# Performance work log

Measured on AMD Instinct MI355X. Metric: run time of the kernel, lower is better.

The kernel has to match this reference:

```python
import jax, jax.numpy as jnp
import numpy as np

EPS = 1e-5  # BatchNorm eps

def _bn(x):
    # BatchNorm1d(affine=False) in training mode: per-agent, per-feature batch stats
    m = jnp.mean(x, axis=1, keepdims=True)
    v = jnp.var(x, axis=1, keepdims=True)
    return (x - m) / jnp.sqrt(v + EPS)

def _lrelu(x):
    return jax.nn.leaky_relu(x, 0.01)

def setup_inputs() -> dict:
    key = jax.random.key(0)
    ks = jax.random.split(key, 14)
    A, B, IN, OUT, H, K = 8, 32768, 128, 32, 128, 4
    D = H // K
    s = 0.05
    return {
        "states": jax.random.normal(ks[0], (A, B, IN), jnp.float32),
        "actions": jax.random.normal(ks[1], (A, B, OUT), jnp.float32),
        "enc_w": jax.random.normal(ks[2], (A, IN + OUT, H), jnp.float32) * s,
        "enc_b": jax.random.normal(ks[3], (A, H), jnp.float32) * s,
        "aenc_w": jax.random.normal(ks[4], (A, OUT, H), jnp.float32) * s,
        "aenc_b": jax.random.normal(ks[5], (A, H), jnp.float32) * s,
        "key_w": jax.random.normal(ks[6], (K, H, D), jnp.float32) * s,
        "sel_w": jax.random.normal(ks[7], (K, H, D), jnp.float32) * s,
        "val_w": jax.random.normal(ks[8], (K, H, D), jnp.float32) * s,
        "val_b": jax.random.normal(ks[9], (K, D), jnp.float32) * s,
        "c1_w": jax.random.normal(ks[10], (A, 2 * H, H), jnp.float32) * s,
        "c1_b": jax.random.normal(ks[11], (A, H), jnp.float32) * s,
        "c2_w": jax.random.normal(ks[12], (A, H, 1), jnp.float32) * s,
        "c2_b": jax.random.normal(ks[13], (A, 1), jnp.float32) * s,
    }

def reference(states, actions, enc_w, enc_b, aenc_w, aenc_b,
              key_w, sel_w, val_w, val_b, c1_w, c1_b, c2_w, c2_b):
    A, B, _ = states.shape
    # per-agent state-action encodings: [A,B,H]
    sa = _bn(jnp.concatenate([states, actions], axis=-1))
    sa_enc = _lrelu(jnp.einsum('abi,aih->abh', sa, enc_w) + enc_b[:, None, :])
    # per-agent action encodings: [A,B,H]
    a_in = _bn(actions)
    a_enc = _lrelu(jnp.einsum('abi,aih->abh', a_in, aenc_w) + aenc_b[:, None, :])
    # per-head keys/values/selectors: [K,A,B,D]
    keys = jnp.einsum('abh,khd->kabd', a_enc, key_w)
    vals = _lrelu(jnp.einsum('abh,khd->kabd', a_enc, val_w) + val_b[:, None, None, :])
    sels = jnp.einsum('abh,khd->kabd', sa_enc, sel_w)
    D = keys.shape[-1]
    # attention logits over other agents: [K,B,A_query,A_key], self excluded
    logits = jnp.einsum('kibd,kjbd->kbij', sels, keys) / jnp.sqrt(jnp.float32(D))
    self_mask = jnp.eye(A, dtype=bool)[None, None]
    probs = jax.nn.softmax(jnp.where(self_mask, -jnp.inf, logits), axis=-1)
    # attended values: [K,A,B,D] -> concat heads -> [A,B,K*D]
    other = jnp.einsum('kbij,kjbd->kibd', probs, vals)
    other_cat = jnp.transpose(other, (1, 2, 0, 3)).reshape(A, B, -1)
    # per-agent critics on [sa_enc, attended]: [A,B,1]
    critic_in = jnp.concatenate([sa_enc, other_cat], axis=-1)
    h = _lrelu(jnp.einsum('abi,aih->abh', critic_in, c1_w) + c1_b[:, None, :])
    q = jnp.einsum('abh,aho->abo', h, c2_w) + c2_b[:, None, :]
    return q
```

## Files before the change

kernel.cpp:

```cpp
#include <hip/hip_runtime.h>
#include <hip/hip_bf16.h>
#include <stdint.h>

#define A_N 8
#define B_N 32768
#define IN_N 128
#define OUT_N 32
#define SAF 160
#define H_N 128
#define D_N 32
#define KD_N 128
#define CIN_N 256
#define CHUNKS 128
#define EPSV 1e-5f
#define ENC_KP 192

typedef unsigned int u32;
typedef unsigned short u16;
typedef __attribute__((ext_vector_type(8))) short short8;
typedef __attribute__((ext_vector_type(4))) float floatx4;

__device__ __forceinline__ float bf_lo(u32 u){ return __uint_as_float(u << 16); }
__device__ __forceinline__ float bf_hi(u32 u){ return __uint_as_float(u & 0xffff0000u); }
__device__ __forceinline__ float bf2f(u16 b){ return __uint_as_float(((u32)b) << 16); }
__device__ __forceinline__ u16 f2bf(float f){
  u32 u = __float_as_uint(f);
  return (u16)((u + 0x7fffu + ((u >> 16) & 1u)) >> 16);
}
__device__ __forceinline__ float lrelu(float x){ return x > 0.f ? x : 0.01f * x; }

__global__ __launch_bounds__(256) void k_stats(
    const float* __restrict__ states, const float* __restrict__ actions,
    float* __restrict__ part)
{
  int a = blockIdx.y;
  int chunk = blockIdx.x;
  int t = threadIdx.x;
  int r0 = chunk * (B_N / CHUNKS);
  __shared__ float red[512];
  {
    int f = t & 127, half = t >> 7;
    const float* p = states + ((size_t)a * B_N + r0 + half) * IN_N + f;
    float s1 = 0.f, s2 = 0.f;
    for (int it = 0; it < 128; ++it){
      float v = p[(size_t)(2 * it) * IN_N];
      s1 += v; s2 += v * v;
    }
    red[t] = s1; red[256 + t] = s2;
    __syncthreads();
    if (t < 128){
      float a1 = red[t] + red[t + 128];
      float a2 = red[256 + t] + red[256 + t + 128];
      size_t o = (((size_t)a * CHUNKS + chunk) * SAF + t) * 2;
      part[o] = a1; part[o + 1] = a2;
    }
    __syncthreads();
  }
  {
    int f = t & 31, g = t >> 5;
    const float* p = actions + ((size_t)a * B_N + r0 + g) * OUT_N + f;
    float s1 = 0.f, s2 = 0.f;
    for (int it = 0; it < 32; ++it){
      float v = p[(size_t)(8 * it) * OUT_N];
      s1 += v; s2 += v * v;
    }
    red[t] = s1; red[256 + t] = s2;
    __syncthreads();
    if (t < 32){
      float a1 = 0.f, a2 = 0.f;
      #pragma unroll
      for (int gg = 0; gg < 8; ++gg){
        a1 += red[t + 32 * gg];
        a2 += red[256 + t + 32 * gg];
      }
      size_t o = (((size_t)a * CHUNKS + chunk) * SAF + 128 + t) * 2;
      part[o] = a1; part[o + 1] = a2;
    }
  }
}

__global__ void k_finalize(const float* __restrict__ part,
                           float* __restrict__ meanArr, float* __restrict__ istdArr)
{
  int idx = blockIdx.x * blockDim.x + threadIdx.x;
  if (idx >= A_N * SAF) return;
  int a = idx / SAF, f = idx % SAF;
  float s1 = 0.f, s2 = 0.f;
  for (int c = 0; c < CHUNKS; ++c){
    size_t o = (((size_t)a * CHUNKS + c) * SAF + f) * 2;
    s1 += part[o]; s2 += part[o + 1];
  }
  float m = s1 * (1.f / B_N);
  float v = s2 * (1.f / B_N) - m * m;
  if (v < 0.f) v = 0.f;
  meanArr[idx] = m;
  istdArr[idx] = rsqrtf(v + EPSV);
}

__device__ __forceinline__ void packpair(float w, u16* __restrict__ dh,
                                         u16* __restrict__ dl, int i){
  u16 h = f2bf(w);
  dh[i] = h;
  dl[i] = f2bf(w - bf2f(h));
}

__global__ __launch_bounds__(256) void k_pack(
    const float* __restrict__ enc_w, const float* __restrict__ aenc_w,
    const float* __restrict__ key_w, const float* __restrict__ sel_w,
    const float* __restrict__ val_w, const float* __restrict__ c1_w,
    u16* __restrict__ encH, u16* __restrict__ encL,
    u16* __restrict__ aencH, u16* __restrict__ aencL,
    u16* __restrict__ keyH, u16* __restrict__ selH, u16* __restrict__ valH,
    u16* __restrict__ c1H, u16* __restrict__ c1L)
{
  int i = blockIdx.x * 256 + threadIdx.x;
  const int S0 = A_N * H_N * ENC_KP;
  const int S1 = A_N * H_N * OUT_N;
  const int S2 = KD_N * H_N;
  const int S5 = A_N * H_N * CIN_N;
  if (i < S0){
    int a = i / (H_N * ENC_KP); int r = i % (H_N * ENC_KP);
    int n = r / ENC_KP; int k = r % ENC_KP;
    float v = (k < SAF) ? enc_w[((size_t)a * SAF + k) * H_N + n] : 0.f;
    packpair(v, encH, encL, i);
    return;
  }
  i -= S0;
  if (i < S1){
    int a = i / (H_N * OUT_N); int r = i % (H_N * OUT_N);
    int n = r / OUT_N; int k = r % OUT_N;
    packpair(aenc_w[((size_t)a * OUT_N + k) * H_N + n], aencH, aencL, i);
    return;
  }
  i -= S1;
  if (i < 3 * S2){
    int which = i / S2; int j = i % S2;
    int n = j / H_N, k = j % H_N;
    const float* w = (which == 0) ? key_w : ((which == 1) ? sel_w : val_w);
    u16* dh = (which == 0) ? keyH : ((which == 1) ? selH : valH);
    dh[j] = f2bf(w[(((size_t)(n >> 5)) * H_N + k) * D_N + (n & 31)]);
    return;
  }
  i -= 3 * S2;
  if (i < S5){
    int a = i / (H_N * CIN_N); int r = i % (H_N * CIN_N);
    int n = r / CIN_N; int k = r % CIN_N;
    packpair(c1_w[((size_t)a * CIN_N + k) * H_N + n], c1H, c1L, i);
  }
}
#define PACK_TOTAL (A_N*H_N*ENC_KP + A_N*H_N*OUT_N + 3*KD_N*H_N + A_N*H_N*CIN_N)

__global__ __launch_bounds__(256, 3) void k_enc_sel(
    const float* __restrict__ states, const float* __restrict__ actions,
    const float* __restrict__ mean, const float* __restrict__ istd,
    const u16* __restrict__ encH, const u16* __restrict__ encL,
    const float* __restrict__ enc_b,
    const u16* __restrict__ selH,
    u16* __restrict__ sa_enc, u16* __restrict__ sels)
{
  int a = blockIdx.y; int row0 = blockIdx.x * 128; int t = threadIdx.x;
  int lane = t & 63, wave = t >> 6, l16 = lane & 15, quad = lane >> 4;
  __shared__ __align__(16) u16 S[22528];
  __shared__ __align__(16) float sc[192], sh[192];
  u16* Wh = S;
  u16* Wl = S + 5120;
  u16* Xh = S + 10240;
  u16* Xl = S + 15360;
  u16* T  = S;
  u16* Ws = S + 17408;

  if (t < 192){
    float m = 0.f, s = 0.f;
    if (t < SAF){ m = mean[a * SAF + t]; s = istd[a * SAF + t]; }
    sc[t] = s; sh[t] = -m * s;
  }
  floatx4 acc[2][8];
  #pragma unroll
  for (int mt = 0; mt < 2; ++mt)
    #pragma unroll
    for (int nt = 0; nt < 8; ++nt) acc[mt][nt] = (floatx4){0.f,0.f,0.f,0.f};
  const u16* wbh = encH + (size_t)a * H_N * ENC_KP;
  const u16* wbl = encL + (size_t)a * H_N * ENC_KP;
  __syncthreads();

  for (int k0 = 0; k0 < ENC_KP; k0 += 32){
    for (int c = t; c < 512; c += 256){
      int n = c >> 2, off = (c & 3) * 8;
      *(uint4*)&Wh[n * 40 + off] = *(const uint4*)(wbh + (size_t)n * ENC_KP + k0 + off);
      *(uint4*)&Wl[n * 40 + off] = *(const uint4*)(wbl + (size_t)n * ENC_KP + k0 + off);
    }
    for (int c = t; c < 1024; c += 256){
      int r = c >> 3, kc = (c & 7) * 4, f = k0 + kc;
      size_t row = (size_t)a * B_N + row0 + r;
      float4 v = {0.f, 0.f, 0.f, 0.f};
      if (f < IN_N)     v = *(const float4*)(states + row * IN_N + f);
      else if (f < SAF) v = *(const float4*)(actions + row * OUT_N + (f - IN_N));
      float4 scv = *(const float4*)&sc[f];
      float4 shv = *(const float4*)&sh[f];
      float x0 = fmaf(v.x, scv.x, shv.x), x1 = fmaf(v.y, scv.y, shv.y);
      float x2 = fmaf(v.z, scv.z, shv.z), x3 = fmaf(v.w, scv.w, shv.w);
      u16 h0 = f2bf(x0), h1 = f2bf(x1), h2 = f2bf(x2), h3 = f2bf(x3);
      *(u32*)&Xh[r * 40 + kc]     = (u32)h0 | ((u32)h1 << 16);
      *(u32*)&Xh[r * 40 + kc + 2] = (u32)h2 | ((u32)h3 << 16);
      u16 l0 = f2bf(x0 - bf2f(h0)), l1 = f2bf(x1 - bf2f(h1));
      u16 l2 = f2bf(x2 - bf2f(h2)), l3 = f2bf(x3 - bf2f(h3));
      *(u32*)&Xl[r * 40 + kc]     = (u32)l0 | ((u32)l1 << 16);
      *(u32*)&Xl[r * 40 + kc + 2] = (u32)l2 | ((u32)l3 << 16);
    }
    __syncthreads();
    {
      short8 ah[2], al[2], bh[8], bl[8];
      #pragma unroll
      for (int mt = 0; mt < 2; ++mt){
        int rr = (wave * 32 + mt * 16 + l16) * 40 + quad * 8;
        ah[mt] = *(const short8*)&Xh[rr];
        al[mt] = *(const short8*)&Xl[rr];
      }
      #pragma unroll
      for (int nt = 0; nt < 8; ++nt){
        int rr = (nt * 16 + l16) * 40 + quad * 8;
        bh[nt] = *(const short8*)&Wh[rr];
        bl[nt] = *(const short8*)&Wl[rr];
      }
      #pragma unroll
      for (int mt = 0; mt < 2; ++mt)
        #pragma unroll
        for (int nt = 0; nt < 8; ++nt){
          acc[mt][nt] = __builtin_amdgcn_mfma_f32_16x16x32_bf16(ah[mt], bh[nt], acc[mt][nt], 0,0,0);
          acc[mt][nt] = __builtin_amdgcn_mfma_f32_16x16x32_bf16(ah[mt], bl[nt], acc[mt][nt], 0,0,0);
          acc[mt][nt] = __builtin_amdgcn_mfma_f32_16x16x32_bf16(al[mt], bh[nt], acc[mt][nt], 0,0,0);
        }
    }
    __syncthreads();
  }

  {
    float bv[8];
    #pragma unroll
    for (int nt = 0; nt < 8; ++nt) bv[nt] = enc_b[a * H_N + nt * 16 + l16];
    #pragma unroll
    for (int mt = 0; mt < 2; ++mt)
      #pragma unroll
      for (int nt = 0; nt < 8; ++nt)
        #pragma unroll
        for (int r = 0; r < 4; ++r){
          int rl = wave * 32 + mt * 16 + quad * 4 + r;
          T[rl * 136 + nt * 16 + l16] = f2bf(lrelu(acc[mt][nt][r] + bv[nt]));
        }
  }
  __syncthreads();
  for (int c = t; c < 2048; c += 256){
    int row = c >> 4, col8 = (c & 15) * 8;
    *(uint4*)(sa_enc + ((size_t)a * B_N + row0 + row) * H_N + col8) =
        *(const uint4*)&T[row * 136 + col8];
  }

  #pragma unroll
  for (int mt = 0; mt < 2; ++mt)
    #pragma unroll
    for (int nt = 0; nt < 8; ++nt) acc[mt][nt] = (floatx4){0.f,0.f,0.f,0.f};
  for (int k0 = 0; k0 < H_N; k0 += 32){
    for (int c = t; c < 512; c += 256){
      int n = c >> 2, off = (c & 3) * 8;
      *(uint4*)&Ws[n * 40 + off] = *(const uint4*)(selH + (size_t)n * H_N + k0 + off);
    }
    __syncthreads();
    {
      short8 ah[2], bh[8];
      #pragma unroll
      for (int mt = 0; mt < 2; ++mt)
        ah[mt] = *(const short8*)&T[(wave * 32 + mt * 16 + l16) * 136 + k0 + quad * 8];
      #pragma unroll
      for (int nt = 0; nt < 8; ++nt)
        bh[nt] = *(const short8*)&Ws[(nt * 16 + l16) * 40 + quad * 8];
      #pragma unroll
      for (int mt = 0; mt < 2; ++mt)
        #pragma unroll
        for (int nt = 0; nt < 8; ++nt)
          acc[mt][nt] = __builtin_amdgcn_mfma_f32_16x16x32_bf16(ah[mt], bh[nt], acc[mt][nt], 0,0,0);
    }
    __syncthreads();
  }
  #pragma unroll
  for (int mt = 0; mt < 2; ++mt)
    #pragma unroll
    for (int nt = 0; nt < 8; ++nt)
      #pragma unroll
      for (int r = 0; r < 4; ++r){
        int rl = wave * 32 + mt * 16 + quad * 4 + r;
        T[rl * 136 + nt * 16 + l16] = f2bf(acc[mt][nt][r]);
      }
  __syncthreads();
  for (int c = t; c < 2048; c += 256){
    int row = c >> 4, col8 = (c & 15) * 8;
    *(uint4*)(sels + ((size_t)a * B_N + row0 + row) * H_N + col8) =
        *(const uint4*)&T[row * 136 + col8];
  }
}

__global__ __launch_bounds__(256, 2) void k_aenc_kv(
    const float* __restrict__ actions,
    const float* __restrict__ mean, const float* __restrict__ istd,
    const u16* __restrict__ aencH, const u16* __restrict__ aencL,
    const float* __restrict__ aenc_b,
    const u16* __restrict__ keyH, const u16* __restrict__ valH,
    const float* __restrict__ val_b,
    u16* __restrict__ keys, u16* __restrict__ vals)
{
  int a = blockIdx.y; int row0 = blockIdx.x * 128; int t = threadIdx.x;
  int lane = t & 63, wave = t >> 6, l16 = lane & 15, quad = lane >> 4;
  __shared__ __align__(16) u16 S[35840];
  __shared__ __align__(16) float sc[32], sh[32];
  u16* T  = S;
  u16* WK = S + 17408;
  u16* WV = S + 26624;
  u16* T2 = S + 17408;

  if (t < 32){
    float m = mean[a * SAF + 128 + t], s = istd[a * SAF + 128 + t];
    sc[t] = s; sh[t] = -m * s;
  }
  floatx4 accK[2][8], accV[2][8];
  #pragma unroll
  for (int mt = 0; mt < 2; ++mt)
    #pragma unroll
    for (int nt = 0; nt < 8; ++nt){
      accK[mt][nt] = (floatx4){0.f,0.f,0.f,0.f};
      accV[mt][nt] = (floatx4){0.f,0.f,0.f,0.f};
    }
  __syncthreads();

  {
    u16* Wh1 = S;  u16* Wl1 = S + 5120;
    u16* Xh = S + 10240; u16* Xl = S + 15360;
    const u16* wbh = aencH + (size_t)a * H_N * OUT_N;
    const u16* wbl = aencL + (size_t)a * H_N * OUT_N;
    for (int c = t; c < 512; c += 256){
      int n = c >> 2, off = (c & 3) * 8;
      *(uint4*)&Wh1[n * 40 + off] = *(const uint4*)(wbh + (size_t)n * OUT_N + off);
      *(uint4*)&Wl1[n * 40 + off] = *(const uint4*)(wbl + (size_t)n * OUT_N + off);
    }
    for (int c = t; c < 1024; c += 256){
      int r = c >> 3, kc = (c & 7) * 4;
      size_t row = (size_t)a * B_N + row0 + r;
      float4 v = *(const float4*)(actions + row * OUT_N + kc);
      float4 scv = *(const float4*)&sc[kc];
      float4 shv = *(const float4*)&sh[kc];
      float x0 = fmaf(v.x, scv.x, shv.x), x1 = fmaf(v.y, scv.y, shv.y);
      float x2 = fmaf(v.z, scv.z, shv.z), x3 = fmaf(v.w, scv.w, shv.w);
      u16 h0 = f2bf(x0), h1 = f2bf(x1), h2 = f2bf(x2), h3 = f2bf(x3);
      *(u32*)&Xh[r * 40 + kc]     = (u32)h0 | ((u32)h1 << 16);
      *(u32*)&Xh[r * 40 + kc + 2] = (u32)h2 | ((u32)h3 << 16);
      u16 l0 = f2bf(x0 - bf2f(h0)), l1 = f2bf(x1 - bf2f(h1));
      u16 l2 = f2bf(x2 - bf2f(h2)), l3 = f2bf(x3 - bf2f(h3));
      *(u32*)&Xl[r * 40 + kc]     = (u32)l0 | ((u32)l1 << 16);
      *(u32*)&Xl[r * 40 + kc + 2] = (u32)l2 | ((u32)l3 << 16);
    }
    __syncthreads();
    short8 ah[2], al[2], bh[8], bl[8];
    #pragma unroll
    for (int mt = 0; mt < 2; ++mt){
      int rr = (wave * 32 + mt * 16 + l16) * 40 + quad * 8;
      ah[mt] = *(const short8*)&Xh[rr];
      al[mt] = *(const short8*)&Xl[rr];
    }
    #pragma unroll
    for (int nt = 0; nt < 8; ++nt){
      int rr = (nt * 16 + l16) * 40 + quad * 8;
      bh[nt] = *(const short8*)&Wh1[rr];
      bl[nt] = *(const short8*)&Wl1[rr];
    }
    #pragma unroll
    for (int mt = 0; mt < 2; ++mt)
      #pragma unroll
      for (int nt = 0; nt < 8; ++nt){
        accK[mt][nt] = __builtin_amdgcn_mfma_f32_16x16x32_bf16(ah[mt], bh[nt], accK[mt][nt], 0,0,0);
        accK[mt][nt] = __builtin_amdgcn_mfma_f32_16x16x32_bf16(ah[mt], bl[nt], accK[mt][nt], 0,0,0);
        accK[mt][nt] = __builtin_amdgcn_mfma_f32_16x16x32_bf16(al[mt], bh[nt], accK[mt][nt], 0,0,0);
      }
    __syncthreads();
  }
  {
    float bv[8];
    #pragma unroll
    for (int nt = 0; nt < 8; ++nt) bv[nt] = aenc_b[a * H_N + nt * 16 + l16];
    #pragma unroll
    for (int mt = 0; mt < 2; ++mt)
      #pragma unroll
      for (int nt = 0; nt < 8; ++nt){
        #pragma unroll
        for (int r = 0; r < 4; ++r){
          int rl = wave * 32 + mt * 16 + quad * 4 + r;
          T[rl * 136 + nt * 16 + l16] = f2bf(lrelu(accK[mt][nt][r] + bv[nt]));
        }
        accK[mt][nt] = (floatx4){0.f,0.f,0.f,0.f};
      }
  }

  for (int k0 = 0; k0 < H_N; k0 += 64){
    __syncthreads();
    for (int c = t; c < 1024; c += 256){
      int n = c >> 3, off = (c & 7) * 8;
      *(uint4*)&WK[n * 72 + off] = *(const uint4*)(keyH + (size_t)n * H_N + k0 + off);
      *(uint4*)&WV[n * 72 + off] = *(const uint4*)(valH + (size_t)n * H_N + k0 + off);
    }
    __syncthreads();
    #pragma unroll
    for (int ks = 0; ks < 64; ks += 32){
      short8 ah[2], bk[8], bv[8];
      #pragma unroll
      for (int mt = 0; mt < 2; ++mt)
        ah[mt] = *(const short8*)&T[(wave * 32 + mt * 16 + l16) * 136 + k0 + ks + quad * 8];
      #pragma unroll
      for (int nt = 0; nt < 8; ++nt){
        int rr = (nt * 16 + l16) * 72 + ks + quad * 8;
        bk[nt] = *(const short8*)&WK[rr];
        bv[nt] = *(const short8*)&WV[rr];
      }
      #pragma unroll
      for (int mt = 0; mt < 2; ++mt)
        #pragma unroll
        for (int nt = 0; nt < 8; ++nt){
          accK[mt][nt] = __builtin_amdgcn_mfma_f32_16x16x32_bf16(ah[mt], bk[nt], accK[mt][nt], 0,0,0);
          accV[mt][nt] = __builtin_amdgcn_mfma_f32_16x16x32_bf16(ah[mt], bv[nt], accV[mt][nt], 0,0,0);
        }
    }
  }
  __syncthreads();
  {
    float bv[8];
    #pragma unroll
    for (int nt = 0; nt < 8; ++nt) bv[nt] = val_b[nt * 16 + l16];
    #pragma unroll
    for (int mt = 0; mt < 2; ++mt)
      #pragma unroll
      for (int nt = 0; nt < 8; ++nt)
        #pragma unroll
        for (int r = 0; r < 4; ++r){
          int rl = wave * 32 + mt * 16 + quad * 4 + r;
          T[rl * 136 + nt * 16 + l16]  = f2bf(lrelu(accV[mt][nt][r] + bv[nt]));
          T2[rl * 136 + nt * 16 + l16] = f2bf(accK[mt][nt][r]);
        }
  }
  __syncthreads();
  for (int c = t; c < 2048; c += 256){
    int row = c >> 4, col8 = (c & 15) * 8;
    *(uint4*)(vals + ((size_t)a * B_N + row0 + row) * H_N + col8) =
        *(const uint4*)&T[row * 136 + col8];
    *(uint4*)(keys + ((size_t)a * B_N + row0 + row) * H_N + col8) =
        *(const uint4*)&T2[row * 136 + col8];
  }
}

__global__ __launch_bounds__(256) void k_attn(
    const u16* __restrict__ sels, const u16* __restrict__ keys,
    const u16* __restrict__ vals, u16* __restrict__ other)
{
  int b0 = blockIdx.x * 8;
  int t = threadIdx.x;
  __shared__ __align__(16) u16 sS[8192], sK[8192], sV[8192];
  u32* dS = (u32*)sS; u32* dK = (u32*)sK; u32* dV = (u32*)sV;
  #pragma unroll
  for (int a = 0; a < 8; ++a){
    size_t go = ((size_t)a * B_N + b0) * KD_N;
    const u32* gs = (const u32*)(sels + go);
    const u32* gk = (const u32*)(keys + go);
    const u32* gv = (const u32*)(vals + go);
    dS[a * 512 + t] = gs[t]; dS[a * 512 + 256 + t] = gs[256 + t];
    dK[a * 512 + t] = gk[t]; dK[a * 512 + 256 + t] = gk[256 + t];
    dV[a * 512 + t] = gv[t]; dV[a * 512 + 256 + t] = gv[256 + t];
  }
  __syncthreads();
  int i = t & 7, p = t >> 3;
  int k = p & 3, bl = p >> 2;
  int base_i = (i * 8 + bl) * 128 + k * 32;
  float si[32];
  {
    const u32* S32 = (const u32*)&sS[base_i];
    #pragma unroll
    for (int d2 = 0; d2 < 16; ++d2){
      u32 u = S32[d2];
      si[2 * d2] = bf_lo(u); si[2 * d2 + 1] = bf_hi(u);
    }
  }
  float lg[8];
  #pragma unroll
  for (int j = 0; j < 8; ++j){
    const u32* K32 = (const u32*)&sK[(j * 8 + bl) * 128 + k * 32];
    float acc = 0.f;
    #pragma unroll
    for (int d2 = 0; d2 < 16; ++d2){
      u32 u = K32[d2];
      acc = fmaf(si[2 * d2], bf_lo(u), acc);
      acc = fmaf(si[2 * d2 + 1], bf_hi(u), acc);
    }
    lg[j] = acc * 0.17677669529663689f;
  }
  float mx = -3.0e38f;
  #pragma unroll
  for (int j = 0; j < 8; ++j) if (j != i) mx = fmaxf(mx, lg[j]);
  float pe[8], se = 0.f;
  #pragma unroll
  for (int j = 0; j < 8; ++j){
    pe[j] = (j == i) ? 0.f : __expf(lg[j] - mx);
    se += pe[j];
  }
  float inv = 1.f / se;
  #pragma unroll
  for (int j = 0; j < 8; ++j) pe[j] *= inv;
  __align__(16) u16 ob[32];
  #pragma unroll
  for (int d2 = 0; d2 < 16; ++d2){
    float acc0 = 0.f, acc1 = 0.f;
    #pragma unroll
    for (int j = 0; j < 8; ++j){
      u32 u = *(const u32*)&sV[(j * 8 + bl) * 128 + k * 32 + 2 * d2];
      acc0 = fmaf(pe[j], bf_lo(u), acc0);
      acc1 = fmaf(pe[j], bf_hi(u), acc1);
    }
    ob[2 * d2] = f2bf(acc0); ob[2 * d2 + 1] = f2bf(acc1);
  }
  uint4* dst = (uint4*)(other + ((size_t)i * B_N + (b0 + bl)) * KD_N + k * 32);
  const uint4* s4 = (const uint4*)ob;
  #pragma unroll
  for (int c = 0; c < 4; ++c) dst[c] = s4[c];
}

__global__ __launch_bounds__(256, 3) void k_critic(
    const u16* __restrict__ sa_enc, const u16* __restrict__ other,
    const u16* __restrict__ c1H, const u16* __restrict__ c1L,
    const float* __restrict__ c1_b,
    const float* __restrict__ c2w, const float* __restrict__ c2b,
    float* __restrict__ qout)
{
  int a = blockIdx.y; int row0 = blockIdx.x * 128; int t = threadIdx.x;
  int lane = t & 63, wave = t >> 6, l16 = lane & 15, quad = lane >> 4;
  __shared__ __align__(16) u16 Xs[5120];
  __shared__ __align__(16) u16 Wh[5120];
  __shared__ __align__(16) u16 Wl[5120];
  floatx4 acc[2][8];
  #pragma unroll
  for (int mt = 0; mt < 2; ++mt)
    #pragma unroll
    for (int nt = 0; nt < 8; ++nt) acc[mt][nt] = (floatx4){0.f,0.f,0.f,0.f};
  const u16* wbh = c1H + (size_t)a * H_N * CIN_N;
  const u16* wbl = c1L + (size_t)a * H_N * CIN_N;

  for (int k0 = 0; k0 < CIN_N; k0 += 32){
    for (int c = t; c < 512; c += 256){
      int n = c >> 2, off = (c & 3) * 8;
      *(uint4*)&Wh[n * 40 + off] = *(const uint4*)(wbh + (size_t)n * CIN_N + k0 + off);
      *(uint4*)&Wl[n * 40 + off] = *(const uint4*)(wbl + (size_t)n * CIN_N + k0 + off);
    }
    for (int c = t; c < 512; c += 256){
      int r = c >> 2, off = (c & 3) * 8;
      int fo = k0 + off;
      const u16* src = sa_enc;
      if (fo >= H_N){ src = other; fo -= H_N; }
      *(uint4*)&Xs[r * 40 + off] =
          *(const uint4*)(src + ((size_t)a * B_N + row0 + r) * H_N + fo);
    }
    __syncthreads();
    {
      short8 ah[2], bh[8], bl[8];
      #pragma unroll
      for (int mt = 0; mt < 2; ++mt)
        ah[mt] = *(const short8*)&Xs[(wave * 32 + mt * 16 + l16) * 40 + quad * 8];
      #pragma unroll
      for (int nt = 0; nt < 8; ++nt){
        int rr = (nt * 16 + l16) * 40 + quad * 8;
        bh[nt] = *(const short8*)&Wh[rr];
        bl[nt] = *(const short8*)&Wl[rr];
      }
      #pragma unroll
      for (int mt = 0; mt < 2; ++mt)
        #pragma unroll
        for (int nt = 0; nt < 8; ++nt){
          acc[mt][nt] = __builtin_amdgcn_mfma_f32_16x16x32_bf16(ah[mt], bh[nt], acc[mt][nt], 0,0,0);
          acc[mt][nt] = __builtin_amdgcn_mfma_f32_16x16x32_bf16(ah[mt], bl[nt], acc[mt][nt], 0,0,0);
        }
    }
    __syncthreads();
  }

  float c2r[8], bv[8];
  #pragma unroll
  for (int nt = 0; nt < 8; ++nt){
    c2r[nt] = c2w[a * H_N + nt * 16 + l16];
    bv[nt]  = c1_b[a * H_N + nt * 16 + l16];
  }
  #pragma unroll
  for (int mt = 0; mt < 2; ++mt){
    #pragma unroll
    for (int r = 0; r < 4; ++r){
      float s = 0.f;
      #pragma unroll
      for (int nt = 0; nt < 8; ++nt){
        float h = lrelu(acc[mt][nt][r] + bv[nt]);
        s = fmaf(h, c2r[nt], s);
      }
      s += __shfl_xor(s, 1);
      s += __shfl_xor(s, 2);
      s += __shfl_xor(s, 4);
      s += __shfl_xor(s, 8);
      if (l16 == 0){
        int row = row0 + wave * 32 + mt * 16 + quad * 4 + r;
        qout[(size_t)a * B_N + row] = s + c2b[a];
      }
    }
  }
}

extern "C" void kernel_launch(void* const* d_in, const int* in_sizes, int n_in,
                              void* d_out, int out_size, void* d_ws, size_t ws_size,
                              hipStream_t stream)
{
  const float* states  = (const float*)d_in[0];
  const float* actions = (const float*)d_in[1];
  const float* enc_w   = (const float*)d_in[2];
  const float* enc_b   = (const float*)d_in[3];
  const float* aenc_w  = (const float*)d_in[4];
  const float* aenc_b  = (const float*)d_in[5];
  const float* key_w   = (const float*)d_in[6];
  const float* sel_w   = (const float*)d_in[7];
  const float* val_w   = (const float*)d_in[8];
  const float* val_b   = (const float*)d_in[9];
  const float* c1_w    = (const float*)d_in[10];
  const float* c1_b    = (const float*)d_in[11];
  const float* c2_w    = (const float*)d_in[12];
  const float* c2_b    = (const float*)d_in[13];
  float* q = (float*)d_out;

  char* ws = (char*)d_ws;
  u16* encH  = (u16*)(ws + 0);
  u16* encL  = (u16*)(ws + 393216);
  u16* aencH = (u16*)(ws + 786432);
  u16* aencL = (u16*)(ws + 851968);
  u16* keyH  = (u16*)(ws + 917504);
  u16* selH  = (u16*)(ws + 950272);
  u16* valH  = (u16*)(ws + 983040);
  float* part    = (float*)ws;
  float* meanArr = (float*)(ws + 1310720);
  float* istdArr = (float*)(ws + 1315840);
  u16* c1H = (u16*)(ws + 1320960);
  u16* c1L = (u16*)(ws + 1845248);
  const size_t ibase = 4194304;
  const size_t BUF = (size_t)A_N * B_N * 128 * 2;
  u16* sa_enc = (u16*)(ws + ibase);
  u16* sels   = (u16*)(ws + ibase + BUF);
  u16* keys   = (u16*)(ws + ibase + 2 * BUF);
  u16* vals   = (u16*)(ws + ibase + 3 * BUF);

  k_stats<<<dim3(CHUNKS, A_N), 256, 0, stream>>>(states, actions, part);
  k_finalize<<<(A_N * SAF + 255) / 256, 256, 0, stream>>>(part, meanArr, istdArr);
  k_pack<<<(PACK_TOTAL + 255) / 256, 256, 0, stream>>>(
      enc_w, aenc_w, key_w, sel_w, val_w, c1_w,
      encH, encL, aencH, aencL, keyH, selH, valH, c1H, c1L);

  dim3 g(B_N / 128, A_N);
  k_enc_sel<<<g, 256, 0, stream>>>(states, actions, meanArr, istdArr,
                                   encH, encL, enc_b, selH, sa_enc, sels);
  k_aenc_kv<<<g, 256, 0, stream>>>(actions, meanArr, istdArr,
                                   aencH, aencL, aenc_b, keyH, valH, val_b,
                                   keys, vals);
  k_attn<<<B_N / 8, 256, 0, stream>>>(sels, keys, vals, keys);
  k_critic<<<g, 256, 0, stream>>>(sa_enc, keys, c1H, c1L, c1_b, c2_w, c2_b, q);
}
```

Baseline: 543.3 us.

## Merge encoder kernels into one role-split launch and register-prefetch global tiles

Replaces the separate state-action/selector and action/key/value kernels with a single launch in which even blocks compute sa_enc and sels while odd blocks compute keys and vals, so both run concurrently and one launch is removed. The K-loops of the encoder and critic GEMMs now load the next tile into registers before the MFMA work on the current tile, hiding global latency behind compute. Key and value projections are now done sequentially in one buffer rather than together, and keys are written straight from accumulators with scattered 2-byte stores. The tradeoffs are higher register pressure and a less coalesced key store path.

```diff
diff --git a/kernel.cpp b/kernel.cpp
--- a/kernel.cpp
+++ b/kernel.cpp
@@ -150,65 +150,238 @@
 }
 #define PACK_TOTAL (A_N*H_N*ENC_KP + A_N*H_N*OUT_N + 3*KD_N*H_N + A_N*H_N*CIN_N)
 
-__global__ __launch_bounds__(256, 3) void k_enc_sel(
+__global__ __launch_bounds__(256, 3) void k_encoders(
     const float* __restrict__ states, const float* __restrict__ actions,
     const float* __restrict__ mean, const float* __restrict__ istd,
     const u16* __restrict__ encH, const u16* __restrict__ encL,
-    const float* __restrict__ enc_b,
-    const u16* __restrict__ selH,
-    u16* __restrict__ sa_enc, u16* __restrict__ sels)
+    const float* __restrict__ enc_b, const u16* __restrict__ selH,
+    const u16* __restrict__ aencH, const u16* __restrict__ aencL,
+    const float* __restrict__ aenc_b,
+    const u16* __restrict__ keyH, const u16* __restrict__ valH,
+    const float* __restrict__ val_b,
+    u16* __restrict__ sa_enc, u16* __restrict__ sels,
+    u16* __restrict__ keys, u16* __restrict__ vals)
 {
-  int a = blockIdx.y; int row0 = blockIdx.x * 128; int t = threadIdx.x;
+  int role = blockIdx.x & 1;
+  int row0 = (blockIdx.x >> 1) * 128;
+  int a = blockIdx.y;
+  int t = threadIdx.x;
   int lane = t & 63, wave = t >> 6, l16 = lane & 15, quad = lane >> 4;
   __shared__ __align__(16) u16 S[22528];
-  __shared__ __align__(16) float sc[192], sh[192];
-  u16* Wh = S;
-  u16* Wl = S + 5120;
-  u16* Xh = S + 10240;
-  u16* Xl = S + 15360;
-  u16* T  = S;
-  u16* Ws = S + 17408;
-
-  if (t < 192){
-    float m = 0.f, s = 0.f;
-    if (t < SAF){ m = mean[a * SAF + t]; s = istd[a * SAF + t]; }
-    sc[t] = s; sh[t] = -m * s;
-  }
+  __shared__ __align__(16) float scsh[384];
+
   floatx4 acc[2][8];
   #pragma unroll
   for (int mt = 0; mt < 2; ++mt)
     #pragma unroll
     for (int nt = 0; nt < 8; ++nt) acc[mt][nt] = (floatx4){0.f,0.f,0.f,0.f};
-  const u16* wbh = encH + (size_t)a * H_N * ENC_KP;
-  const u16* wbl = encL + (size_t)a * H_N * ENC_KP;
-  __syncthreads();
-
-  for (int k0 = 0; k0 < ENC_KP; k0 += 32){
-    for (int c = t; c < 512; c += 256){
-      int n = c >> 2, off = (c & 3) * 8;
-      *(uint4*)&Wh[n * 40 + off] = *(const uint4*)(wbh + (size_t)n * ENC_KP + k0 + off);
-      *(uint4*)&Wl[n * 40 + off] = *(const uint4*)(wbl + (size_t)n * ENC_KP + k0 + off);
-    }
-    for (int c = t; c < 1024; c += 256){
-      int r = c >> 3, kc = (c & 7) * 4, f = k0 + kc;
-      size_t row = (size_t)a * B_N + row0 + r;
-      float4 v = {0.f, 0.f, 0.f, 0.f};
-      if (f < IN_N)     v = *(const float4*)(states + row * IN_N + f);
-      else if (f < SAF) v = *(const float4*)(actions + row * OUT_N + (f - IN_N));
-      float4 scv = *(const float4*)&sc[f];
-      float4 shv = *(const float4*)&sh[f];
-      float x0 = fmaf(v.x, scv.x, shv.x), x1 = fmaf(v.y, scv.y, shv.y);
-      float x2 = fmaf(v.z, scv.z, shv.z), x3 = fmaf(v.w, scv.w, shv.w);
-      u16 h0 = f2bf(x0), h1 = f2bf(x1), h2 = f2bf(x2), h3 = f2bf(x3);
-      *(u32*)&Xh[r * 40 + kc]     = (u32)h0 | ((u32)h1 << 16);
-      *(u32*)&Xh[r * 40 + kc + 2] = (u32)h2 | ((u32)h3 << 16);
-      u16 l0 = f2bf(x0 - bf2f(h0)), l1 = f2bf(x1 - bf2f(h1));
-      u16 l2 = f2bf(x2 - bf2f(h2)), l3 = f2bf(x3 - bf2f(h3));
-      *(u32*)&Xl[r * 40 + kc]     = (u32)l0 | ((u32)l1 << 16);
-      *(u32*)&Xl[r * 40 + kc + 2] = (u32)l2 | ((u32)l3 << 16);
-    }
-    __syncthreads();
+
+  if (role == 0){
+    u16* Wh = S;
+    u16* Wl = S + 5120;
+    u16* Xh = S + 10240;
+    u16* Xl = S + 15360;
+    u16* T  = S;
+    u16* Ws2 = S + 17408;
+    float* sc = scsh; float* sh = scsh + 192;
+
+    if (t < 192){
+      float m = 0.f, s = 0.f;
+      if (t < SAF){ m = mean[a * SAF + t]; s = istd[a * SAF + t]; }
+      sc[t] = s; sh[t] = -m * s;
+    }
+    const u16* wbh = encH + (size_t)a * H_N * ENC_KP;
+    const u16* wbl = encL + (size_t)a * H_N * ENC_KP;
+    __syncthreads();
+
+    uint4 pwh[2], pwl[2]; float4 px[4];
+    auto loadW = [&](int k0){
+      #pragma unroll
+      for (int i = 0; i < 2; ++i){
+        int c = t + i * 256; int n = c >> 2, off = (c & 3) * 8;
+        pwh[i] = *(const uint4*)(wbh + (size_t)n * ENC_KP + k0 + off);
+        pwl[i] = *(const uint4*)(wbl + (size_t)n * ENC_KP + k0 + off);
+      }
+    };
+    auto loadX = [&](int k0){
+      #pragma unroll
+      for (int i = 0; i < 4; ++i){
+        int c = t + i * 256; int r = c >> 3, kc = (c & 7) * 4, f = k0 + kc;
+        size_t row = (size_t)a * B_N + row0 + r;
+        float4 v = {0.f, 0.f, 0.f, 0.f};
+        if (f < IN_N)     v = *(const float4*)(states + row * IN_N + f);
+        else if (f < SAF) v = *(const float4*)(actions + row * OUT_N + (f - IN_N));
+        px[i] = v;
+      }
+    };
+    auto storeTiles = [&](int k0){
+      #pragma unroll
+      for (int i = 0; i < 2; ++i){
+        int c = t + i * 256; int n = c >> 2, off = (c & 3) * 8;
+        *(uint4*)&Wh[n * 40 + off] = pwh[i];
+        *(uint4*)&Wl[n * 40 + off] = pwl[i];
+      }
+      #pragma unroll
+      for (int i = 0; i < 4; ++i){
+        int c = t + i * 256; int r = c >> 3, kc = (c & 7) * 4, f = k0 + kc;
+        float4 v = px[i];
+        float4 scv = *(const float4*)&sc[f];
+        float4 shv = *(const float4*)&sh[f];
+        float x0 = fmaf(v.x, scv.x, shv.x), x1 = fmaf(v.y, scv.y, shv.y);
+        float x2 = fmaf(v.z, scv.z, shv.z), x3 = fmaf(v.w, scv.w, shv.w);
+        u16 h0 = f2bf(x0), h1 = f2bf(x1), h2 = f2bf(x2), h3 = f2bf(x3);
+        *(u32*)&Xh[r * 40 + kc]     = (u32)h0 | ((u32)h1 << 16);
+        *(u32*)&Xh[r * 40 + kc + 2] = (u32)h2 | ((u32)h3 << 16);
+        u16 l0 = f2bf(x0 - bf2f(h0)), l1 = f2bf(x1 - bf2f(h1));
+        u16 l2 = f2bf(x2 - bf2f(h2)), l3 = f2bf(x3 - bf2f(h3));
+        *(u32*)&Xl[r * 40 + kc]     = (u32)l0 | ((u32)l1 << 16);
+        *(u32*)&Xl[r * 40 + kc + 2] = (u32)l2 | ((u32)l3 << 16);
+      }
+    };
+
+    loadW(0); loadX(0);
+    for (int k0 = 0; k0 < ENC_KP; k0 += 32){
+      storeTiles(k0);
+      __syncthreads();
+      if (k0 + 32 < ENC_KP){ loadW(k0 + 32); loadX(k0 + 32); }
+      {
+        short8 ah[2], al[2], bh[8], bl[8];
+        #pragma unroll
+        for (int mt = 0; mt < 2; ++mt){
+          int rr = (wave * 32 + mt * 16 + l16) * 40 + quad * 8;
+          ah[mt] = *(const short8*)&Xh[rr];
+          al[mt] = *(const short8*)&Xl[rr];
+        }
+        #pragma unroll
+        for (int nt = 0; nt < 8; ++nt){
+          int rr = (nt * 16 + l16) * 40 + quad * 8;
+          bh[nt] = *(const short8*)&Wh[rr];
+          bl[nt] = *(const short8*)&Wl[rr];
+        }
+        #pragma unroll
+        for (int mt = 0; mt < 2; ++mt)
+          #pragma unroll
+          for (int nt = 0; nt < 8; ++nt){
+            acc[mt][nt] = __builtin_amdgcn_mfma_f32_16x16x32_bf16(ah[mt], bh[nt], acc[mt][nt], 0,0,0);
+            acc[mt][nt] = __builtin_amdgcn_mfma_f32_16x16x32_bf16(ah[mt], bl[nt], acc[mt][nt], 0,0,0);
+            acc[mt][nt] = __builtin_amdgcn_mfma_f32_16x16x32_bf16(al[mt], bh[nt], acc[mt][nt], 0,0,0);
+          }
+      }
+      __syncthreads();
+    }
+
     {
+      float bv[8];
+      #pragma unroll
+      for (int nt = 0; nt < 8; ++nt) bv[nt] = enc_b[a * H_N + nt * 16 + l16];
+      #pragma unroll
+      for (int mt = 0; mt < 2; ++mt)
+        #pragma unroll
+        for (int nt = 0; nt < 8; ++nt)
+          #pragma unroll
+          for (int r = 0; r < 4; ++r){
+            int rl = wave * 32 + mt * 16 + quad * 4 + r;
+            T[rl * 136 + nt * 16 + l16] = f2bf(lrelu(acc[mt][nt][r] + bv[nt]));
+          }
+    }
+    __syncthreads();
+    for (int c = t; c < 2048; c += 256){
+      int row = c >> 4, col8 = (c & 15) * 8;
+      *(uint4*)(sa_enc + ((size_t)a * B_N + row0 + row) * H_N + col8) =
+          *(const uint4*)&T[row * 136 + col8];
+    }
+
+    #pragma unroll
+    for (int mt = 0; mt < 2; ++mt)
+      #pragma unroll
+      for (int nt = 0; nt < 8; ++nt) acc[mt][nt] = (floatx4){0.f,0.f,0.f,0.f};
+    uint4 ps[2];
+    auto loadS = [&](int k0){
+      #pragma unroll
+      for (int i = 0; i < 2; ++i){
+        int c = t + i * 256; int n = c >> 2, off = (c & 3) * 8;
+        ps[i] = *(const uint4*)(selH + (size_t)n * H_N + k0 + off);
+      }
+    };
+    loadS(0);
+    for (int k0 = 0; k0 < H_N; k0 += 32){
+      #pragma unroll
+      for (int i = 0; i < 2; ++i){
+        int c = t + i * 256; int n = c >> 2, off = (c & 3) * 8;
+        *(uint4*)&Ws2[n * 40 + off] = ps[i];
+      }
+      __syncthreads();
+      if (k0 + 32 < H_N) loadS(k0 + 32);
+      {
+        short8 ah[2], bh[8];
+        #pragma unroll
+        for (int mt = 0; mt < 2; ++mt)
+          ah[mt] = *(const short8*)&T[(wave * 32 + mt * 16 + l16) * 136 + k0 + quad * 8];
+        #pragma unroll
+        for (int nt = 0; nt < 8; ++nt)
+          bh[nt] = *(const short8*)&Ws2[(nt * 16 + l16) * 40 + quad * 8];
+        #pragma unroll
+        for (int mt = 0; mt < 2; ++mt)
+          #pragma unroll
+          for (int nt = 0; nt < 8; ++nt)
+            acc[mt][nt] = __builtin_amdgcn_mfma_f32_16x16x32_bf16(ah[mt], bh[nt], acc[mt][nt], 0,0,0);
+      }
+      __syncthreads();
+    }
+    #pragma unroll
+    for (int mt = 0; mt < 2; ++mt)
+      #pragma unroll
+      for (int nt = 0; nt < 8; ++nt)
+        #pragma unroll
+        for (int r = 0; r < 4; ++r){
+          int rl = wave * 32 + mt * 16 + quad * 4 + r;
+          T[rl * 136 + nt * 16 + l16] = f2bf(acc[mt][nt][r]);
+        }
+    __syncthreads();
+    for (int c = t; c < 2048; c += 256){
+      int row = c >> 4, col8 = (c & 15) * 8;
+      *(uint4*)(sels + ((size_t)a * B_N + row0 + row) * H_N + col8) =
+          *(const uint4*)&T[row * 136 + col8];
+    }
+
+  } else {
+    u16* T = S;
+    u16* W2 = S + 17408;
+    float* sc = scsh; float* sh = scsh + 32;
+
+    if (t < 32){
+      float m = mean[a * SAF + 128 + t], s = istd[a * SAF + 128 + t];
+      sc[t] = s; sh[t] = -m * s;
+    }
+    __syncthreads();
+
+    {
+      u16* Wh1 = S;  u16* Wl1 = S + 5120;
+      u16* Xh = S + 10240; u16* Xl = S + 15360;
+      const u16* wbh = aencH + (size_t)a * H_N * OUT_N;
+      const u16* wbl = aencL + (size_t)a * H_N * OUT_N;
+      for (int c = t; c < 512; c += 256){
+        int n = c >> 2, off = (c & 3) * 8;
+        *(uint4*)&Wh1[n * 40 + off] = *(const uint4*)(wbh + (size_t)n * OUT_N + off);
+        *(uint4*)&Wl1[n * 40 + off] = *(const uint4*)(wbl + (size_t)n * OUT_N + off);
+      }
+      for (int c = t; c < 1024; c += 256){
+        int r = c >> 3, kc = (c & 7) * 4;
+        size_t row = (size_t)a * B_N + row0 + r;
+        float4 v = *(const float4*)(actions + row * OUT_N + kc);
+        float4 scv = *(const float4*)&sc[kc];
+        float4 shv = *(const float4*)&sh[kc];
+        float x0 = fmaf(v.x, scv.x, shv.x), x1 = fmaf(v.y, scv.y, shv.y);
+        float x2 = fmaf(v.z, scv.z, shv.z), x3 = fmaf(v.w, scv.w, shv.w);
+        u16 h0 = f2bf(x0), h1 = f2bf(x1), h2 = f2bf(x2), h3 = f2bf(x3);
+        *(u32*)&Xh[r * 40 + kc]     = (u32)h0 | ((u32)h1 << 16);
+        *(u32*)&Xh[r * 40 + kc + 2] = (u32)h2 | ((u32)h3 << 16);
+        u16 l0 = f2bf(x0 - bf2f(h0)), l1 = f2bf(x1 - bf2f(h1));
+        u16 l2 = f2bf(x2 - bf2f(h2)), l3 = f2bf(x3 - bf2f(h3));
+        *(u32*)&Xl[r * 40 + kc]     = (u32)l0 | ((u32)l1 << 16);
+        *(u32*)&Xl[r * 40 + kc + 2] = (u32)l2 | ((u32)l3 << 16);
+      }
+      __syncthreads();
       short8 ah[2], al[2], bh[8], bl[8];
       #pragma unroll
       for (int mt = 0; mt < 2; ++mt){
@@ -219,8 +392,8 @@
       #pragma unroll
       for (int nt = 0; nt < 8; ++nt){
         int rr = (nt * 16 + l16) * 40 + quad * 8;
-        bh[nt] = *(const short8*)&Wh[rr];
-        bl[nt] = *(const short8*)&Wl[rr];
+        bh[nt] = *(const short8*)&Wh1[rr];
+        bl[nt] = *(const short8*)&Wl1[rr];
       }
       #pragma unroll
       for (int mt = 0; mt < 2; ++mt)
@@ -230,225 +403,97 @@
           acc[mt][nt] = __builtin_amdgcn_mfma_f32_16x16x32_bf16(ah[mt], bl[nt], acc[mt][nt], 0,0,0);
           acc[mt][nt] = __builtin_amdgcn_mfma_f32_16x16x32_bf16(al[mt], bh[nt], acc[mt][nt], 0,0,0);
         }
-    }
-    __syncthreads();
-  }
-
-  {
-    float bv[8];
-    #pragma unroll
-    for (int nt = 0; nt < 8; ++nt) bv[nt] = enc_b[a * H_N + nt * 16 + l16];
-    #pragma unroll
-    for (int mt = 0; mt < 2; ++mt)
-      #pragma unroll
-      for (int nt = 0; nt < 8; ++nt)
-        #pragma unroll
-        for (int r = 0; r < 4; ++r){
-          int rl = wave * 32 + mt * 16 + quad * 4 + r;
-          T[rl * 136 + nt * 16 + l16] = f2bf(lrelu(acc[mt][nt][r] + bv[nt]));
+      __syncthreads();
+    }
+    {
+      float bv[8];
+      #pragma unroll
+      for (int nt = 0; nt < 8; ++nt) bv[nt] = aenc_b[a * H_N + nt * 16 + l16];
+      #pragma unroll
+      for (int mt = 0; mt < 2; ++mt)
+        #pragma unroll
+        for (int nt = 0; nt < 8; ++nt){
+          #pragma unroll
+          for (int r = 0; r < 4; ++r){
+            int rl = wave * 32 + mt * 16 + quad * 4 + r;
+            T[rl * 136 + nt * 16 + l16] = f2bf(lrelu(acc[mt][nt][r] + bv[nt]));
+          }
         }
-  }
-  __syncthreads();
-  for (int c = t; c < 2048; c += 256){
-    int row = c >> 4, col8 = (c & 15) * 8;
-    *(uint4*)(sa_enc + ((size_t)a * B_N + row0 + row) * H_N + col8) =
-        *(const uint4*)&T[row * 136 + col8];
-  }
-
-  #pragma unroll
-  for (int mt = 0; mt < 2; ++mt)
-    #pragma unroll
-    for (int nt = 0; nt < 8; ++nt) acc[mt][nt] = (floatx4){0.f,0.f,0.f,0.f};
-  for (int k0 = 0; k0 < H_N; k0 += 32){
-    for (int c = t; c < 512; c += 256){
-      int n = c >> 2, off = (c & 3) * 8;
-      *(uint4*)&Ws[n * 40 + off] = *(const uint4*)(selH + (size_t)n * H_N + k0 + off);
-    }
-    __syncthreads();
+    }
+
+    uint4 pw[2];
+    auto loadW2 = [&](const u16* wsrc, int k0){
+      #pragma unroll
+      for (int i = 0; i < 2; ++i){
+        int c = t + i * 256; int n = c >> 2, off = (c & 3) * 8;
+        pw[i] = *(const uint4*)(wsrc + (size_t)n * H_N + k0 + off);
+      }
+    };
+    #pragma unroll
+    for (int ph = 0; ph < 2; ++ph){
+      const u16* wsrc = (ph == 0) ? keyH : valH;
+      #pragma unroll
+      for (int mt = 0; mt < 2; ++mt)
+        #pragma unroll
+        for (int nt = 0; nt < 8; ++nt) acc[mt][nt] = (floatx4){0.f,0.f,0.f,0.f};
+      loadW2(wsrc, 0);
+      for (int k0 = 0; k0 < H_N; k0 += 32){
+        #pragma unroll
+        for (int i = 0; i < 2; ++i){
+          int c = t + i * 256; int n = c >> 2, off = (c & 3) * 8;
+          *(uint4*)&W2[n * 40 + off] = pw[i];
+        }
+        __syncthreads();
+        if (k0 + 32 < H_N) loadW2(wsrc, k0 + 32);
+        {
+          short8 ah[2], bh[8];
+          #pragma unroll
+          for (int mt = 0; mt < 2; ++mt)
+            ah[mt] = *(const short8*)&T[(wave * 32 + mt * 16 + l16) * 136 + k0 + quad * 8];
+          #pragma unroll
+          for (int nt = 0; nt < 8; ++nt)
+            bh[nt] = *(const short8*)&W2[(nt * 16 + l16) * 40 + quad * 8];
+          #pragma unroll
+          for (int mt = 0; mt < 2; ++mt)
+            #pragma unroll
+            for (int nt = 0; nt < 8; ++nt)
+              acc[mt][nt] = __builtin_amdgcn_mfma_f32_16x16x32_bf16(ah[mt], bh[nt], acc[mt][nt], 0,0,0);
+        }
+        __syncthreads();
+      }
+      if (ph == 0){
+        #pragma unroll
+        for (int mt = 0; mt < 2; ++mt)
+          #pragma unroll
+          for (int nt = 0; nt < 8; ++nt)
+            #pragma unroll
+            for (int r = 0; r < 4; ++r){
+              int rl = wave * 32 + mt * 16 + quad * 4 + r;
+              keys[((size_t)a * B_N + row0 + rl) * H_N + nt * 16 + l16] =
+                  f2bf(acc[mt][nt][r]);
+            }
+      }
+    }
     {
-      short8 ah[2], bh[8];
+      float bv[8];
+      #pragma unroll
+      for (int nt = 0; nt < 8; ++nt) bv[nt] = val_b[nt * 16 + l16];
       #pragma unroll
       for (int mt = 0; mt < 2; ++mt)
-        ah[mt] = *(const short8*)&T[(wave * 32 + mt * 16 + l16) * 136 + k0 + quad * 8];
-      #pragma unroll
-      for (int nt = 0; nt < 8; ++nt)
-        bh[nt] = *(const short8*)&Ws[(nt * 16 + l16) * 40 + quad * 8];
-      #pragma unroll
-      for (int mt = 0; mt < 2; ++mt)
         #pragma unroll
         for (int nt = 0; nt < 8; ++nt)
-          acc[mt][nt] = __builtin_amdgcn_mfma_f32_16x16x32_bf16(ah[mt], bh[nt], acc[mt][nt], 0,0,0);
-    }
-    __syncthreads();
-  }
-  #pragma unroll
-  for (int mt = 0; mt < 2; ++mt)
-    #pragma unroll
-    for (int nt = 0; nt < 8; ++nt)
-      #pragma unroll
-      for (int r = 0; r < 4; ++r){
-        int rl = wave * 32 + mt * 16 + quad * 4 + r;
-        T[rl * 136 + nt * 16 + l16] = f2bf(acc[mt][nt][r]);
-      }
-  __syncthreads();
-  for (int c = t; c < 2048; c += 256){
-    int row = c >> 4, col8 = (c & 15) * 8;
-    *(uint4*)(sels + ((size_t)a * B_N + row0 + row) * H_N + col8) =
-        *(const uint4*)&T[row * 136 + col8];
-  }
-}
-
-__global__ __launch_bounds__(256, 2) void k_aenc_kv(
-    const float* __restrict__ actions,
-    const float* __restrict__ mean, const float* __restrict__ istd,
-    const u16* __restrict__ aencH, const u16* __restrict__ aencL,
-    const float* __restrict__ aenc_b,
-    const u16* __restrict__ keyH, const u16* __restrict__ valH,
-    const float* __restrict__ val_b,
-    u16* __restrict__ keys, u16* __restrict__ vals)
-{
-  int a = blockIdx.y; int row0 = blockIdx.x * 128; int t = threadIdx.x;
-  int lane = t & 63, wave = t >> 6, l16 = lane & 15, quad = lane >> 4;
-  __shared__ __align__(16) u16 S[35840];
-  __shared__ __align__(16) float sc[32], sh[32];
-  u16* T  = S;
-  u16* WK = S + 17408;
-  u16* WV = S + 26624;
-  u16* T2 = S + 17408;
-
-  if (t < 32){
-    float m = mean[a * SAF + 128 + t], s = istd[a * SAF + 128 + t];
-    sc[t] = s; sh[t] = -m * s;
-  }
-  floatx4 accK[2][8], accV[2][8];
-  #pragma unroll
-  for (int mt = 0; mt < 2; ++mt)
-    #pragma unroll
-    for (int nt = 0; nt < 8; ++nt){
-      accK[mt][nt] = (floatx4){0.f,0.f,0.f,0.f};
-      accV[mt][nt] = (floatx4){0.f,0.f,0.f,0.f};
-    }
-  __syncthreads();
-
-  {
-    u16* Wh1 = S;  u16* Wl1 = S + 5120;
-    u16* Xh = S + 10240; u16* Xl = S + 15360;
-    const u16* wbh = aencH + (size_t)a * H_N * OUT_N;
-    const u16* wbl = aencL + (size_t)a * H_N * OUT_N;
-    for (int c = t; c < 512; c += 256){
-      int n = c >> 2, off = (c & 3) * 8;
-      *(uint4*)&Wh1[n * 40 + off] = *(const uint4*)(wbh + (size_t)n * OUT_N + off);
-      *(uint4*)&Wl1[n * 40 + off] = *(const uint4*)(wbl + (size_t)n * OUT_N + off);
-    }
-    for (int c = t; c < 1024; c += 256){
-      int r = c >> 3, kc = (c & 7) * 4;
-      size_t row = (size_t)a * B_N + row0 + r;
-      float4 v = *(const float4*)(actions + row * OUT_N + kc);
-      float4 scv = *(const float4*)&sc[kc];
-      float4 shv = *(const float4*)&sh[kc];
-      float x0 = fmaf(v.x, scv.x, shv.x), x1 = fmaf(v.y, scv.y, shv.y);
-      float x2 = fmaf(v.z, scv.z, shv.z), x3 = fmaf(v.w, scv.w, shv.w);
-      u16 h0 = f2bf(x0), h1 = f2bf(x1), h2 = f2bf(x2), h3 = f2bf(x3);
-      *(u32*)&Xh[r * 40 + kc]     = (u32)h0 | ((u32)h1 << 16);
-      *(u32*)&Xh[r * 40 + kc + 2] = (u32)h2 | ((u32)h3 << 16);
-      u16 l0 = f2bf(x0 - bf2f(h0)), l1 = f2bf(x1 - bf2f(h1));
-      u16 l2 = f2bf(x2 - bf2f(h2)), l3 = f2bf(x3 - bf2f(h3));
-      *(u32*)&Xl[r * 40 + kc]     = (u32)l0 | ((u32)l1 << 16);
-      *(u32*)&Xl[r * 40 + kc + 2] = (u32)l2 | ((u32)l3 << 16);
-    }
-    __syncthreads();
-    short8 ah[2], al[2], bh[8], bl[8];
-    #pragma unroll
-    for (int mt = 0; mt < 2; ++mt){
-      int rr = (wave * 32 + mt * 16 + l16) * 40 + quad * 8;
-      ah[mt] = *(const short8*)&Xh[rr];
-      al[mt] = *(const short8*)&Xl[rr];
-    }
-    #pragma unroll
-    for (int nt = 0; nt < 8; ++nt){
-      int rr = (nt * 16 + l16) * 40 + quad * 8;
-      bh[nt] = *(const short8*)&Wh1[rr];
-      bl[nt] = *(const short8*)&Wl1[rr];
-    }
-    #pragma unroll
-    for (int mt = 0; mt < 2; ++mt)
-      #pragma unroll
-      for (int nt = 0; nt < 8; ++nt){
-        accK[mt][nt] = __builtin_amdgcn_mfma_f32_16x16x32_bf16(ah[mt], bh[nt], accK[mt][nt], 0,0,0);
-        accK[mt][nt] = __builtin_amdgcn_mfma_f32_16x16x32_bf16(ah[mt], bl[nt], accK[mt][nt], 0,0,0);
-        accK[mt][nt] = __builtin_amdgcn_mfma_f32_16x16x32_bf16(al[mt], bh[nt], accK[mt][nt], 0,0,0);
-      }
-    __syncthreads();
-  }
-  {
-    float bv[8];
-    #pragma unroll
-    for (int nt = 0; nt < 8; ++nt) bv[nt] = aenc_b[a * H_N + nt * 16 + l16];
-    #pragma unroll
-    for (int mt = 0; mt < 2; ++mt)
-      #pragma unroll
-      for (int nt = 0; nt < 8; ++nt){
-        #pragma unroll
-        for (int r = 0; r < 4; ++r){
-          int rl = wave * 32 + mt * 16 + quad * 4 + r;
-          T[rl * 136 + nt * 16 + l16] = f2bf(lrelu(accK[mt][nt][r] + bv[nt]));
-        }
-        accK[mt][nt] = (floatx4){0.f,0.f,0.f,0.f};
-      }
-  }
-
-  for (int k0 = 0; k0 < H_N; k0 += 64){
-    __syncthreads();
-    for (int c = t; c < 1024; c += 256){
-      int n = c >> 3, off = (c & 7) * 8;
-      *(uint4*)&WK[n * 72 + off] = *(const uint4*)(keyH + (size_t)n * H_N + k0 + off);
-      *(uint4*)&WV[n * 72 + off] = *(const uint4*)(valH + (size_t)n * H_N + k0 + off);
-    }
-    __syncthreads();
-    #pragma unroll
-    for (int ks = 0; ks < 64; ks += 32){
-      short8 ah[2], bk[8], bv[8];
-      #pragma unroll
-      for (int mt = 0; mt < 2; ++mt)
-        ah[mt] = *(const short8*)&T[(wave * 32 + mt * 16 + l16) * 136 + k0 + ks + quad * 8];
-      #pragma unroll
-      for (int nt = 0; nt < 8; ++nt){
-        int rr = (nt * 16 + l16) * 72 + ks + quad * 8;
-        bk[nt] = *(const short8*)&WK[rr];
-        bv[nt] = *(const short8*)&WV[rr];
-      }
-      #pragma unroll
-      for (int mt = 0; mt < 2; ++mt)
-        #pragma unroll
-        for (int nt = 0; nt < 8; ++nt){
-          accK[mt][nt] = __builtin_amdgcn_mfma_f32_16x16x32_bf16(ah[mt], bk[nt], accK[mt][nt], 0,0,0);
-          accV[mt][nt] = __builtin_amdgcn_mfma_f32_16x16x32_bf16(ah[mt], bv[nt], accV[mt][nt], 0,0,0);
-        }
-    }
-  }
-  __syncthreads();
-  {
-    float bv[8];
-    #pragma unroll
-    for (int nt = 0; nt < 8; ++nt) bv[nt] = val_b[nt * 16 + l16];
-    #pragma unroll
-    for (int mt = 0; mt < 2; ++mt)
-      #pragma unroll
-      for (int nt = 0; nt < 8; ++nt)
-        #pragma unroll
-        for (int r = 0; r < 4; ++r){
-          int rl = wave * 32 + mt * 16 + quad * 4 + r;
-          T[rl * 136 + nt * 16 + l16]  = f2bf(lrelu(accV[mt][nt][r] + bv[nt]));
-          T2[rl * 136 + nt * 16 + l16] = f2bf(accK[mt][nt][r]);
-        }
-  }
-  __syncthreads();
-  for (int c = t; c < 2048; c += 256){
-    int row = c >> 4, col8 = (c & 15) * 8;
-    *(uint4*)(vals + ((size_t)a * B_N + row0 + row) * H_N + col8) =
-        *(const uint4*)&T[row * 136 + col8];
-    *(uint4*)(keys + ((size_t)a * B_N + row0 + row) * H_N + col8) =
-        *(const uint4*)&T2[row * 136 + col8];
+          #pragma unroll
+          for (int r = 0; r < 4; ++r){
+            int rl = wave * 32 + mt * 16 + quad * 4 + r;
+            T[rl * 136 + nt * 16 + l16] = f2bf(lrelu(acc[mt][nt][r] + bv[nt]));
+          }
+    }
+    __syncthreads();
+    for (int c = t; c < 2048; c += 256){
+      int row = c >> 4, col8 = (c & 15) * 8;
+      *(uint4*)(vals + ((size_t)a * B_N + row0 + row) * H_N + col8) =
+          *(const uint4*)&T[row * 136 + col8];
+    }
   }
 }
 
@@ -546,21 +591,36 @@
   const u16* wbh = c1H + (size_t)a * H_N * CIN_N;
   const u16* wbl = c1L + (size_t)a * H_N * CIN_N;
 
-  for (int k0 = 0; k0 < CIN_N; k0 += 32){
-    for (int c = t; c < 512; c += 256){
-      int n = c >> 2, off = (c & 3) * 8;
-      *(uint4*)&Wh[n * 40 + off] = *(const uint4*)(wbh + (size_t)n * CIN_N + k0 + off);
-      *(uint4*)&Wl[n * 40 + off] = *(const uint4*)(wbl + (size_t)n * CIN_N + k0 + off);
-    }
-    for (int c = t; c < 512; c += 256){
-      int r = c >> 2, off = (c & 3) * 8;
+  uint4 pwh[2], pwl[2], pxr[2];
+  auto ldW = [&](int k0){
+    #pragma unroll
+    for (int i = 0; i < 2; ++i){
+      int c = t + i * 256; int n = c >> 2, off = (c & 3) * 8;
+      pwh[i] = *(const uint4*)(wbh + (size_t)n * CIN_N + k0 + off);
+      pwl[i] = *(const uint4*)(wbl + (size_t)n * CIN_N + k0 + off);
+    }
+  };
+  auto ldX = [&](int k0){
+    #pragma unroll
+    for (int i = 0; i < 2; ++i){
+      int c = t + i * 256; int r = c >> 2, off = (c & 3) * 8;
       int fo = k0 + off;
       const u16* src = sa_enc;
       if (fo >= H_N){ src = other; fo -= H_N; }
-      *(uint4*)&Xs[r * 40 + off] =
-          *(const uint4*)(src + ((size_t)a * B_N + row0 + r) * H_N + fo);
-    }
-    __syncthreads();
+      pxr[i] = *(const uint4*)(src + ((size_t)a * B_N + row0 + r) * H_N + fo);
+    }
+  };
+  ldW(0); ldX(0);
+  for (int k0 = 0; k0 < CIN_N; k0 += 32){
+    #pragma unroll
+    for (int i = 0; i < 2; ++i){
+      int c = t + i * 256; int n = c >> 2, off = (c & 3) * 8;
+      *(uint4*)&Wh[n * 40 + off] = pwh[i];
+      *(uint4*)&Wl[n * 40 + off] = pwl[i];
+      *(uint4*)&Xs[n * 40 + off] = pxr[i];
+    }
+    __syncthreads();
+    if (k0 + 32 < CIN_N){ ldW(k0 + 32); ldX(k0 + 32); }
     {
       short8 ah[2], bh[8], bl[8];
       #pragma unroll
@@ -657,12 +717,12 @@
       enc_w, aenc_w, key_w, sel_w, val_w, c1_w,
       encH, encL, aencH, aencL, keyH, selH, valH, c1H, c1L);
 
-  dim3 g(B_N / 128, A_N);
-  k_enc_sel<<<g, 256, 0, stream>>>(states, actions, meanArr, istdArr,
-                                   encH, encL, enc_b, selH, sa_enc, sels);
-  k_aenc_kv<<<g, 256, 0, stream>>>(actions, meanArr, istdArr,
-                                   aencH, aencL, aenc_b, keyH, valH, val_b,
-                                   keys, vals);
+  k_encoders<<<dim3(B_N / 128 * 2, A_N), 256, 0, stream>>>(
+      states, actions, meanArr, istdArr,
+      encH, encL, enc_b, selH,
+      aencH, aencL, aenc_b, keyH, valH, val_b,
+      sa_enc, sels, keys, vals);
   k_attn<<<B_N / 8, 256, 0, stream>>>(sels, keys, vals, keys);
-  k_critic<<<g, 256, 0, stream>>>(sa_enc, keys, c1H, c1L, c1_b, c2_w, c2_b, q);
-}
+  k_critic<<<dim3(B_N / 128, A_N), 256, 0, stream>>>(
+      sa_enc, keys, c1H, c1L, c1_b, c2_w, c2_b, q);
+}
```

Result: slower. 768.1 us (+41.4%).
